# Kernel optimization log

Measured on AMD Instinct MI355X. Metric: run time of the kernel, lower is better.

The kernel has to match this reference:

```python
import jax, jax.numpy as jnp
import numpy as np

N = 100000   # subcomplex cells (nodes)
E = 600000   # edges in high-adjacency subcomplex graph
NB = 50000   # bridge (rank-0) cells
C = 128      # input_channels
H = 128      # hidden_channels
BN_EPS = 1e-5


def setup_inputs() -> dict:
    key = jax.random.key(0)
    ks = jax.random.split(key, 12)
    x = jax.random.normal(ks[0], (N, C), jnp.float32)
    x0 = jax.random.normal(ks[1], (NB, C), jnp.float32)
    edge_index = jax.random.randint(ks[2], (2, E), 0, N)
    bridge_index = jax.random.randint(ks[3], (E,), 0, NB)
    s1 = 1.0 / np.sqrt(C)
    s2 = 1.0 / np.sqrt(H)
    W1 = jax.random.uniform(ks[4], (C, H), jnp.float32, -s1, s1)
    b1 = jax.random.uniform(ks[5], (H,), jnp.float32, -s1, s1)
    W2 = jax.random.uniform(ks[6], (H, H), jnp.float32, -s2, s2)
    b2 = jax.random.uniform(ks[7], (H,), jnp.float32, -s2, s2)
    gamma1 = jnp.ones((H,), jnp.float32)
    beta1 = jnp.zeros((H,), jnp.float32)
    gamma2 = jnp.ones((H,), jnp.float32)
    beta2 = jnp.zeros((H,), jnp.float32)
    eps_gin = jnp.zeros((), jnp.float32)  # GIN train_eps, init 0
    return {"x": x, "x0": x0, "edge_index": edge_index, "bridge_index": bridge_index,
            "W1": W1, "b1": b1, "gamma1": gamma1, "beta1": beta1,
            "W2": W2, "b2": b2, "gamma2": gamma2, "beta2": beta2,
            "eps_gin": eps_gin}


def _bn(h, gamma, beta):
    # BatchNorm1d in training mode: batch stats over node dim, biased var
    mu = jnp.mean(h, axis=0)
    var = jnp.mean((h - mu) ** 2, axis=0)
    return gamma * (h - mu) * jax.lax.rsqrt(var + BN_EPS) + beta


def reference(x, x0, edge_index, bridge_index, W1, b1, gamma1, beta1,
              W2, b2, gamma2, beta2, eps_gin):
    src, dst = edge_index[0], edge_index[1]
    # edge attributes: gather bridge-cell features per edge  [E, C]
    edge_attr = x0[bridge_index]
    # GINE-style message: relu(x_j + e_ij), scatter-add into destination
    msg = jax.nn.relu(x[src] + edge_attr)
    aggr = jax.ops.segment_sum(msg, dst, num_segments=x.shape[0])  # [N, C]
    h = (1.0 + eps_gin) * x + aggr
    # 2-layer MLP: Linear -> BN -> ReLU, twice
    h = jax.nn.relu(_bn(h @ W1 + b1, gamma1, beta1))
    h = jax.nn.relu(_bn(h @ W2 + b2, gamma2, beta2))
    return h
```

## Files before the change

kernel.cpp:

```cpp
#include <hip/hip_runtime.h>


typedef __attribute__((ext_vector_type(8))) short bf16x8;
typedef __attribute__((ext_vector_type(4))) float floatx4;

__device__ __forceinline__ unsigned short f2bf(float f) {
  unsigned u = __float_as_uint(f);
  u += 0x7fff + ((u >> 16) & 1);
  return (unsigned short)(u >> 16);
}
__device__ __forceinline__ unsigned pk2(float a, float b) {
  return (unsigned)f2bf(a) | ((unsigned)f2bf(b) << 16);
}
__device__ __forceinline__ float bflo(unsigned u) { return __uint_as_float(u << 16); }
__device__ __forceinline__ float bfhi(unsigned u) { return __uint_as_float(u & 0xffff0000u); }

__global__ __launch_bounds__(256) void k_front(
    const float* __restrict__ x, const float* __restrict__ x0,
    const float* __restrict__ W1, const float* __restrict__ W2,
    unsigned short* __restrict__ WT1, unsigned short* __restrict__ WT2,
    uint4* __restrict__ zbase, int zitems, int zblocks,
    uint4* __restrict__ xb, int nx,
    uint4* __restrict__ x0b, int nx0) {
  int b = blockIdx.x;
  int tid = threadIdx.x;
  if (b < 2) {
    const float* W = b ? W2 : W1;
    unsigned short* WT = b ? WT2 : WT1;
#pragma unroll
    for (int i = 0; i < 16; ++i) {
      int g = tid + i * 256;
      int k = g >> 5;
      int n0 = (g & 31) * 4;
      float4 v = *(const float4*)(W + k * 128 + n0);
      WT[(n0 + 0) * 128 + k] = f2bf(v.x);
      WT[(n0 + 1) * 128 + k] = f2bf(v.y);
      WT[(n0 + 2) * 128 + k] = f2bf(v.z);
      WT[(n0 + 3) * 128 + k] = f2bf(v.w);
    }
    return;
  }
  if (b < 2 + zblocks) {
    int t = (b - 2) * 256 + tid;
    if (t < zitems) zbase[t] = make_uint4(0, 0, 0, 0);
    return;
  }
  int t = (b - 2 - zblocks) * 256 + tid;
  const float* s;
  uint4* d;
  if (t < nx) { s = x + (size_t)t * 8; d = xb + t; }
  else {
    t -= nx;
    if (t >= nx0) return;
    s = x0 + (size_t)t * 8; d = x0b + t;
  }
  float4 a = *(const float4*)s;
  float4 c = *(const float4*)(s + 4);
  uint4 o;
  o.x = pk2(a.x, a.y); o.y = pk2(a.z, a.w);
  o.z = pk2(c.x, c.y); o.w = pk2(c.z, c.w);
  *d = o;
}

__global__ __launch_bounds__(256) void k_scatter(
    const int* __restrict__ src, const int* __restrict__ dst,
    const int* __restrict__ bri, int* __restrict__ cnt,
    int2* __restrict__ slots, int E_) {
  int e = blockIdx.x * 256 + threadIdx.x;
  if (e >= E_) return;
  int d = dst[e];
  int pos = atomicAdd(&cnt[d], 1);
  if (pos < 32) slots[d * 32 + pos] = make_int2(src[e], bri[e]);
}

__global__ __launch_bounds__(256) void k_aggr(
    const uint4* __restrict__ xb, const uint4* __restrict__ x0b,
    const int* __restrict__ cnt, const int2* __restrict__ slots,
    const float* __restrict__ eps, uint4* __restrict__ aggr, int n) {
  int tid = threadIdx.x;
  int node = blockIdx.x * 32 + (tid >> 3);
  if (node >= n) return;
  int q = (tid & 7) + blockIdx.y * 8;
  float s = 1.0f + eps[0];
  float acc[8];
  uint4 xi = xb[(size_t)node * 16 + q];
  acc[0] = s * bflo(xi.x); acc[1] = s * bfhi(xi.x);
  acc[2] = s * bflo(xi.y); acc[3] = s * bfhi(xi.y);
  acc[4] = s * bflo(xi.z); acc[5] = s * bfhi(xi.z);
  acc[6] = s * bflo(xi.w); acc[7] = s * bfhi(xi.w);
  int end = cnt[node];
  if (end > 32) end = 32;
  int base = node * 32;
  for (int j = 0; j < end; ++j) {
    int2 p = slots[base + j];
    uint4 xa = xb[(size_t)p.x * 16 + q];
    uint4 ea = x0b[(size_t)p.y * 16 + q];
    acc[0] += fmaxf(bflo(xa.x) + bflo(ea.x), 0.f);
    acc[1] += fmaxf(bfhi(xa.x) + bfhi(ea.x), 0.f);
    acc[2] += fmaxf(bflo(xa.y) + bflo(ea.y), 0.f);
    acc[3] += fmaxf(bfhi(xa.y) + bfhi(ea.y), 0.f);
    acc[4] += fmaxf(bflo(xa.z) + bflo(ea.z), 0.f);
    acc[5] += fmaxf(bfhi(xa.z) + bfhi(ea.z), 0.f);
    acc[6] += fmaxf(bflo(xa.w) + bflo(ea.w), 0.f);
    acc[7] += fmaxf(bfhi(xa.w) + bfhi(ea.w), 0.f);
  }
  uint4 o;
  o.x = pk2(acc[0], acc[1]); o.y = pk2(acc[2], acc[3]);
  o.z = pk2(acc[4], acc[5]); o.w = pk2(acc[6], acc[7]);
  aggr[(size_t)node * 16 + q] = o;
}

__global__ __launch_bounds__(256) void k_gemmb(
    const unsigned short* A, const unsigned short* __restrict__ WT,
    const float* __restrict__ bias,
    const float* __restrict__ psum, const float* __restrict__ psq,
    const float* __restrict__ gam, const float* __restrict__ bet,
    unsigned short* Out,
    float* __restrict__ osum, float* __restrict__ osq,
    int nrows, float inv_n, int fuse) {
  __shared__ unsigned short LDSraw[128 * 144];
  unsigned short* As = LDSraw;
  unsigned short* Bs = LDSraw + 128 * 72;
  __shared__ float sL[128], hL[128];
  int tid = threadIdx.x;
  if (fuse && tid < 128) {
    float mu = psum[tid] * inv_n;
    float var = psq[tid] * inv_n - mu * mu;
    float rs = rsqrtf(var + 1e-5f);
    float sc = gam[tid] * rs;
    sL[tid] = sc;
    hL[tid] = bet[tid] - mu * sc;
  }
  __syncthreads();

  int row0 = blockIdx.x * 128;
  int lane = tid & 63;
  int wid = tid >> 6;
  int wr = (wid >> 1) * 64;
  int wc = (wid & 1) * 64;
  int lr = lane & 15;
  int quad = lane >> 4;

  floatx4 acc[4][4];
#pragma unroll
  for (int mi = 0; mi < 4; ++mi)
#pragma unroll
    for (int ni = 0; ni < 4; ++ni) acc[mi][ni] = (floatx4)0.0f;

  for (int kc = 0; kc < 128; kc += 64) {
    if (kc) __syncthreads();
#pragma unroll
    for (int i = 0; i < 4; ++i) {
      int g = tid + i * 256;
      int r = g >> 3;
      int c8 = g & 7;
      int row = row0 + r;
      uint4 v = make_uint4(0, 0, 0, 0);
      if (row < nrows)
        v = *(const uint4*)(A + (size_t)row * 128 + kc + c8 * 8);
      if (fuse) {
        int k = kc + c8 * 8;
        v.x = pk2(fmaxf(fmaf(sL[k + 0], bflo(v.x), hL[k + 0]), 0.f),
                  fmaxf(fmaf(sL[k + 1], bfhi(v.x), hL[k + 1]), 0.f));
        v.y = pk2(fmaxf(fmaf(sL[k + 2], bflo(v.y), hL[k + 2]), 0.f),
                  fmaxf(fmaf(sL[k + 3], bfhi(v.y), hL[k + 3]), 0.f));
        v.z = pk2(fmaxf(fmaf(sL[k + 4], bflo(v.z), hL[k + 4]), 0.f),
                  fmaxf(fmaf(sL[k + 5], bfhi(v.z), hL[k + 5]), 0.f));
        v.w = pk2(fmaxf(fmaf(sL[k + 6], bflo(v.w), hL[k + 6]), 0.f),
                  fmaxf(fmaf(sL[k + 7], bfhi(v.w), hL[k + 7]), 0.f));
      }
      *(uint4*)&As[r * 72 + c8 * 8] = v;
    }
#pragma unroll
    for (int i = 0; i < 4; ++i) {
      int g = tid + i * 256;
      int nn = g >> 3;
      int c8 = g & 7;
      *(uint4*)&Bs[nn * 72 + c8 * 8] =
          *(const uint4*)(WT + (size_t)nn * 128 + kc + c8 * 8);
    }
    __syncthreads();
#pragma unroll
    for (int ks = 0; ks < 2; ++ks) {
      int k0 = ks * 32 + quad * 8;
      bf16x8 af[4], bfr[4];
#pragma unroll
      for (int mi = 0; mi < 4; ++mi)
        af[mi] = *(const bf16x8*)&As[(wr + mi * 16 + lr) * 72 + k0];
#pragma unroll
      for (int ni = 0; ni < 4; ++ni)
        bfr[ni] = *(const bf16x8*)&Bs[(wc + ni * 16 + lr) * 72 + k0];
#pragma unroll
      for (int mi = 0; mi < 4; ++mi)
#pragma unroll
        for (int ni = 0; ni < 4; ++ni)
          acc[mi][ni] = __builtin_amdgcn_mfma_f32_16x16x32_bf16(
              af[mi], bfr[ni], acc[mi][ni], 0, 0, 0);
    }
  }
  __syncthreads();

  float bv[4];
#pragma unroll
  for (int ni = 0; ni < 4; ++ni) bv[ni] = bias[wc + ni * 16 + lr];
  float s_sum[4] = {0.f, 0.f, 0.f, 0.f};
  float s_sq[4]  = {0.f, 0.f, 0.f, 0.f};
#pragma unroll
  for (int mi = 0; mi < 4; ++mi) {
#pragma unroll
    for (int r = 0; r < 4; ++r) {
      int rl = wr + mi * 16 + quad * 4 + r;
      bool ok = (row0 + rl) < nrows;
#pragma unroll
      for (int ni = 0; ni < 4; ++ni) {
        int col = wc + ni * 16 + lr;
        float v = acc[mi][ni][r] + bv[ni];
        LDSraw[rl * 136 + col] = f2bf(v);
        if (ok) { s_sum[ni] += v; s_sq[ni] += v * v; }
      }
    }
  }
#pragma unroll
  for (int ni = 0; ni < 4; ++ni) {
    s_sum[ni] += __shfl_xor(s_sum[ni], 16, 64);
    s_sum[ni] += __shfl_xor(s_sum[ni], 32, 64);
    s_sq[ni]  += __shfl_xor(s_sq[ni], 16, 64);
    s_sq[ni]  += __shfl_xor(s_sq[ni], 32, 64);
  }
  if (quad == 0) {
#pragma unroll
    for (int ni = 0; ni < 4; ++ni) {
      int col = wc + ni * 16 + lr;
      unsafeAtomicAdd(&osum[col], s_sum[ni]);
      unsafeAtomicAdd(&osq[col], s_sq[ni]);
    }
  }
  __syncthreads();
#pragma unroll
  for (int i = 0; i < 8; ++i) {
    int g = tid + i * 256;
    int r = g >> 4;
    int c8 = g & 15;
    if (row0 + r < nrows)
      *(uint4*)(Out + (size_t)(row0 + r) * 128 + c8 * 8) =
          *(const uint4*)&LDSraw[r * 136 + c8 * 8];
  }
}

__global__ __launch_bounds__(256) void k_bnrelu(
    const uint4* __restrict__ h, const float* __restrict__ psum,
    const float* __restrict__ psq, const float* __restrict__ gam,
    const float* __restrict__ bet, float* __restrict__ out,
    int items, float inv_n) {
  __shared__ float sL[128], hL[128];
  int tid = threadIdx.x;
  if (tid < 128) {
    float mu = psum[tid] * inv_n;
    float var = psq[tid] * inv_n - mu * mu;
    float rs = rsqrtf(var + 1e-5f);
    float sc = gam[tid] * rs;
    sL[tid] = sc;
    hL[tid] = bet[tid] - mu * sc;
  }
  __syncthreads();
  int t = blockIdx.x * 256 + tid;
  if (t >= items) return;
  int c = (t & 15) * 8;
  uint4 v = h[t];
  float4 o1, o2;
  o1.x = fmaxf(fmaf(sL[c + 0], bflo(v.x), hL[c + 0]), 0.f);
  o1.y = fmaxf(fmaf(sL[c + 1], bfhi(v.x), hL[c + 1]), 0.f);
  o1.z = fmaxf(fmaf(sL[c + 2], bflo(v.y), hL[c + 2]), 0.f);
  o1.w = fmaxf(fmaf(sL[c + 3], bfhi(v.y), hL[c + 3]), 0.f);
  o2.x = fmaxf(fmaf(sL[c + 4], bflo(v.z), hL[c + 4]), 0.f);
  o2.y = fmaxf(fmaf(sL[c + 5], bfhi(v.z), hL[c + 5]), 0.f);
  o2.z = fmaxf(fmaf(sL[c + 6], bflo(v.w), hL[c + 6]), 0.f);
  o2.w = fmaxf(fmaf(sL[c + 7], bfhi(v.w), hL[c + 7]), 0.f);
  ((float4*)out)[(size_t)t * 2 + 0] = o1;
  ((float4*)out)[(size_t)t * 2 + 1] = o2;
}

extern "C" void kernel_launch(void* const* d_in, const int* in_sizes, int n_in,
                              void* d_out, int out_size, void* d_ws, size_t ws_size,
                              hipStream_t stream) {
  const float* x   = (const float*)d_in[0];
  const float* x0  = (const float*)d_in[1];
  const int*   ei  = (const int*)d_in[2];
  const int*   bi  = (const int*)d_in[3];
  const float* W1  = (const float*)d_in[4];
  const float* b1  = (const float*)d_in[5];
  const float* g1  = (const float*)d_in[6];
  const float* be1 = (const float*)d_in[7];
  const float* W2  = (const float*)d_in[8];
  const float* b2  = (const float*)d_in[9];
  const float* g2  = (const float*)d_in[10];
  const float* be2 = (const float*)d_in[11];
  const float* eps = (const float*)d_in[12];

  int N  = in_sizes[0] / 128;
  int NB = in_sizes[1] / 128;
  int E_ = in_sizes[3];
  const int* srcp = ei;
  const int* dstp = ei + E_;

  int2* slots = (int2*)d_ws;
  int* cnt    = (int*)(slots + (size_t)N * 32);
  float* stats = (float*)(cnt + N);
  float* sum1 = stats;       float* sq1 = stats + 128;
  float* sum2 = stats + 256; float* sq2 = stats + 384;
  unsigned short* WT1  = (unsigned short*)(stats + 512);
  unsigned short* WT2  = WT1 + 16384;
  unsigned short* abuf = WT2 + 16384;

  unsigned short* xb  = (unsigned short*)d_out;
  unsigned short* x0b = xb + (size_t)N * 128;

  int zitems  = (N + 512 + 3) / 4;
  int zblocks = (zitems + 255) / 256;
  int nx  = N * 16;
  int nx0 = NB * 16;
  int cvtblocks = (nx + nx0 + 255) / 256;
  float inv_n = 1.0f / (float)N;

  k_front<<<2 + zblocks + cvtblocks, 256, 0, stream>>>(
      x, x0, W1, W2, WT1, WT2, (uint4*)cnt, zitems, zblocks,
      (uint4*)xb, nx, (uint4*)x0b, nx0);

  k_scatter<<<(E_ + 255) / 256, 256, 0, stream>>>(srcp, dstp, bi, cnt,
                                                  slots, E_);

  dim3 agrid((N * 8 + 255) / 256, 2);
  k_aggr<<<agrid, 256, 0, stream>>>(
      (const uint4*)xb, (const uint4*)x0b, cnt, slots, eps,
      (uint4*)abuf, N);

  int gblocks = (N + 127) / 128;
  k_gemmb<<<gblocks, 256, 0, stream>>>(abuf, WT1, b1, nullptr, nullptr,
                                       nullptr, nullptr, abuf, sum1, sq1,
                                       N, inv_n, 0);
  k_gemmb<<<gblocks, 256, 0, stream>>>(abuf, WT2, b2, sum1, sq1, g1, be1,
                                       abuf, sum2, sq2, N, inv_n, 1);

  k_bnrelu<<<(N * 16 + 255) / 256, 256, 0, stream>>>(
      (const uint4*)abuf, sum2, sq2, g2, be2, (float*)d_out, N * 16, inv_n);
}
```

Measured before the change: 343.6 us.

## Fuse all stages into one persistent cooperative kernel with grid syncs

Replaces the six separate launches (convert/zero, scatter, aggregate, two GEMMs, final BN-ReLU) with one cooperative persistent kernel. The kernel loops over work with grid-stride and separates phases with grid.sync(). The goal is to remove launch gaps and tail effects between small kernels. In exchange, grid size is capped by occupancy, each phase loses some parallelism, and every phase boundary pays a grid-wide barrier. The aggregation also changes from two half-row blocks to 16 threads per node.

```diff
diff --git a/kernel.cpp b/kernel.cpp
--- a/kernel.cpp
+++ b/kernel.cpp
@@ -1,4 +1,7 @@
 #include <hip/hip_runtime.h>
+#include <hip/hip_cooperative_groups.h>
+
+namespace cg = cooperative_groups;
 
 
 typedef __attribute__((ext_vector_type(8))) short bf16x8;
@@ -15,125 +18,31 @@
 __device__ __forceinline__ float bflo(unsigned u) { return __uint_as_float(u << 16); }
 __device__ __forceinline__ float bfhi(unsigned u) { return __uint_as_float(u & 0xffff0000u); }
 
-__global__ __launch_bounds__(256) void k_front(
-    const float* __restrict__ x, const float* __restrict__ x0,
-    const float* __restrict__ W1, const float* __restrict__ W2,
-    unsigned short* __restrict__ WT1, unsigned short* __restrict__ WT2,
-    uint4* __restrict__ zbase, int zitems, int zblocks,
-    uint4* __restrict__ xb, int nx,
-    uint4* __restrict__ x0b, int nx0) {
-  int b = blockIdx.x;
-  int tid = threadIdx.x;
-  if (b < 2) {
-    const float* W = b ? W2 : W1;
-    unsigned short* WT = b ? WT2 : WT1;
-#pragma unroll
-    for (int i = 0; i < 16; ++i) {
-      int g = tid + i * 256;
-      int k = g >> 5;
-      int n0 = (g & 31) * 4;
-      float4 v = *(const float4*)(W + k * 128 + n0);
-      WT[(n0 + 0) * 128 + k] = f2bf(v.x);
-      WT[(n0 + 1) * 128 + k] = f2bf(v.y);
-      WT[(n0 + 2) * 128 + k] = f2bf(v.z);
-      WT[(n0 + 3) * 128 + k] = f2bf(v.w);
-    }
-    return;
-  }
-  if (b < 2 + zblocks) {
-    int t = (b - 2) * 256 + tid;
-    if (t < zitems) zbase[t] = make_uint4(0, 0, 0, 0);
-    return;
-  }
-  int t = (b - 2 - zblocks) * 256 + tid;
-  const float* s;
-  uint4* d;
-  if (t < nx) { s = x + (size_t)t * 8; d = xb + t; }
-  else {
-    t -= nx;
-    if (t >= nx0) return;
-    s = x0 + (size_t)t * 8; d = x0b + t;
-  }
-  float4 a = *(const float4*)s;
-  float4 c = *(const float4*)(s + 4);
-  uint4 o;
-  o.x = pk2(a.x, a.y); o.y = pk2(a.z, a.w);
-  o.z = pk2(c.x, c.y); o.w = pk2(c.z, c.w);
-  *d = o;
-}
-
-__global__ __launch_bounds__(256) void k_scatter(
-    const int* __restrict__ src, const int* __restrict__ dst,
-    const int* __restrict__ bri, int* __restrict__ cnt,
-    int2* __restrict__ slots, int E_) {
-  int e = blockIdx.x * 256 + threadIdx.x;
-  if (e >= E_) return;
-  int d = dst[e];
-  int pos = atomicAdd(&cnt[d], 1);
-  if (pos < 32) slots[d * 32 + pos] = make_int2(src[e], bri[e]);
-}
-
-__global__ __launch_bounds__(256) void k_aggr(
-    const uint4* __restrict__ xb, const uint4* __restrict__ x0b,
-    const int* __restrict__ cnt, const int2* __restrict__ slots,
-    const float* __restrict__ eps, uint4* __restrict__ aggr, int n) {
-  int tid = threadIdx.x;
-  int node = blockIdx.x * 32 + (tid >> 3);
-  if (node >= n) return;
-  int q = (tid & 7) + blockIdx.y * 8;
-  float s = 1.0f + eps[0];
-  float acc[8];
-  uint4 xi = xb[(size_t)node * 16 + q];
-  acc[0] = s * bflo(xi.x); acc[1] = s * bfhi(xi.x);
-  acc[2] = s * bflo(xi.y); acc[3] = s * bfhi(xi.y);
-  acc[4] = s * bflo(xi.z); acc[5] = s * bfhi(xi.z);
-  acc[6] = s * bflo(xi.w); acc[7] = s * bfhi(xi.w);
-  int end = cnt[node];
-  if (end > 32) end = 32;
-  int base = node * 32;
-  for (int j = 0; j < end; ++j) {
-    int2 p = slots[base + j];
-    uint4 xa = xb[(size_t)p.x * 16 + q];
-    uint4 ea = x0b[(size_t)p.y * 16 + q];
-    acc[0] += fmaxf(bflo(xa.x) + bflo(ea.x), 0.f);
-    acc[1] += fmaxf(bfhi(xa.x) + bfhi(ea.x), 0.f);
-    acc[2] += fmaxf(bflo(xa.y) + bflo(ea.y), 0.f);
-    acc[3] += fmaxf(bfhi(xa.y) + bfhi(ea.y), 0.f);
-    acc[4] += fmaxf(bflo(xa.z) + bflo(ea.z), 0.f);
-    acc[5] += fmaxf(bfhi(xa.z) + bfhi(ea.z), 0.f);
-    acc[6] += fmaxf(bflo(xa.w) + bflo(ea.w), 0.f);
-    acc[7] += fmaxf(bfhi(xa.w) + bfhi(ea.w), 0.f);
-  }
-  uint4 o;
-  o.x = pk2(acc[0], acc[1]); o.y = pk2(acc[2], acc[3]);
-  o.z = pk2(acc[4], acc[5]); o.w = pk2(acc[6], acc[7]);
-  aggr[(size_t)node * 16 + q] = o;
-}
-
-__global__ __launch_bounds__(256) void k_gemmb(
-    const unsigned short* A, const unsigned short* __restrict__ WT,
-    const float* __restrict__ bias,
-    const float* __restrict__ psum, const float* __restrict__ psq,
-    const float* __restrict__ gam, const float* __restrict__ bet,
-    unsigned short* Out,
-    float* __restrict__ osum, float* __restrict__ osq,
-    int nrows, float inv_n, int fuse) {
-  __shared__ unsigned short LDSraw[128 * 144];
+struct MegaParams {
+  const float *x, *x0;
+  const int *src, *dst, *bri;
+  const float *W1, *b1, *g1, *be1;
+  const float *W2, *b2, *g2, *be2;
+  const float *eps;
+  unsigned short *xb, *x0b, *WT1, *WT2, *abuf;
+  int2 *slots;
+  int *cnt;
+  float *stats;
+  uint4 *zbase;
+  int zitems;
+  float *out;
+  int N, NB, E;
+  float inv_n;
+};
+
+__device__ __forceinline__ void gemm_tile(
+    int t, int tid, const unsigned short* A, const unsigned short* WT,
+    const float* bias, unsigned short* Out, float* osum, float* osq,
+    int nrows, unsigned short* LDSraw, const float* sL, const float* hL,
+    int fuse) {
   unsigned short* As = LDSraw;
   unsigned short* Bs = LDSraw + 128 * 72;
-  __shared__ float sL[128], hL[128];
-  int tid = threadIdx.x;
-  if (fuse && tid < 128) {
-    float mu = psum[tid] * inv_n;
-    float var = psq[tid] * inv_n - mu * mu;
-    float rs = rsqrtf(var + 1e-5f);
-    float sc = gam[tid] * rs;
-    sL[tid] = sc;
-    hL[tid] = bet[tid] - mu * sc;
-  }
-  __syncthreads();
-
-  int row0 = blockIdx.x * 128;
+  int row0 = t << 7;
   int lane = tid & 63;
   int wid = tid >> 6;
   int wr = (wid >> 1) * 64;
@@ -147,8 +56,9 @@
 #pragma unroll
     for (int ni = 0; ni < 4; ++ni) acc[mi][ni] = (floatx4)0.0f;
 
+#pragma unroll
   for (int kc = 0; kc < 128; kc += 64) {
-    if (kc) __syncthreads();
+    __syncthreads();
 #pragma unroll
     for (int i = 0; i < 4; ++i) {
       int g = tid + i * 256;
@@ -247,13 +157,10 @@
   }
 }
 
-__global__ __launch_bounds__(256) void k_bnrelu(
-    const uint4* __restrict__ h, const float* __restrict__ psum,
-    const float* __restrict__ psq, const float* __restrict__ gam,
-    const float* __restrict__ bet, float* __restrict__ out,
-    int items, float inv_n) {
-  __shared__ float sL[128], hL[128];
-  int tid = threadIdx.x;
+__device__ __forceinline__ void fold_bn(int tid, const float* psum,
+                                        const float* psq, const float* gam,
+                                        const float* bet, float inv_n,
+                                        float* sL, float* hL) {
   if (tid < 128) {
     float mu = psum[tid] * inv_n;
     float var = psq[tid] * inv_n - mu * mu;
@@ -262,85 +169,170 @@
     sL[tid] = sc;
     hL[tid] = bet[tid] - mu * sc;
   }
+}
+
+__global__ __launch_bounds__(256, 3) void k_mega(MegaParams p) {
+  cg::grid_group grid = cg::this_grid();
+  __shared__ unsigned short LDSraw[128 * 144];
+  __shared__ float sL[128], hL[128];
+  int tid = threadIdx.x;
+  int gid = blockIdx.x * 256 + tid;
+  int gsize = gridDim.x * 256;
+
+  for (int i = gid; i < p.zitems; i += gsize) p.zbase[i] = make_uint4(0, 0, 0, 0);
+  int nx = p.N * 16;
+  for (int i = gid; i < nx; i += gsize) {
+    const float* s = p.x + (size_t)i * 8;
+    float4 a = *(const float4*)s;
+    float4 c = *(const float4*)(s + 4);
+    uint4 o;
+    o.x = pk2(a.x, a.y); o.y = pk2(a.z, a.w);
+    o.z = pk2(c.x, c.y); o.w = pk2(c.z, c.w);
+    ((uint4*)p.xb)[i] = o;
+  }
+  int nx0 = p.NB * 16;
+  for (int i = gid; i < nx0; i += gsize) {
+    const float* s = p.x0 + (size_t)i * 8;
+    float4 a = *(const float4*)s;
+    float4 c = *(const float4*)(s + 4);
+    uint4 o;
+    o.x = pk2(a.x, a.y); o.y = pk2(a.z, a.w);
+    o.z = pk2(c.x, c.y); o.w = pk2(c.z, c.w);
+    ((uint4*)p.x0b)[i] = o;
+  }
+  for (int i = gid; i < 8192; i += gsize) {
+    const float* W = (i & 4096) ? p.W2 : p.W1;
+    unsigned short* WT = (i & 4096) ? p.WT2 : p.WT1;
+    int r = i & 4095;
+    int k = r >> 5;
+    int n0 = (r & 31) * 4;
+    float4 v = *(const float4*)(W + k * 128 + n0);
+    WT[(n0 + 0) * 128 + k] = f2bf(v.x);
+    WT[(n0 + 1) * 128 + k] = f2bf(v.y);
+    WT[(n0 + 2) * 128 + k] = f2bf(v.z);
+    WT[(n0 + 3) * 128 + k] = f2bf(v.w);
+  }
+  grid.sync();
+
+  for (int e = gid; e < p.E; e += gsize) {
+    int d = p.dst[e];
+    int pos = atomicAdd(&p.cnt[d], 1);
+    if (pos < 32) p.slots[d * 32 + pos] = make_int2(p.src[e], p.bri[e]);
+  }
+  grid.sync();
+
+  {
+    float epsv = 1.0f + p.eps[0];
+    int q = tid & 15;
+    int ngroups = gsize >> 4;
+    for (int n = (gid >> 4); n < p.N; n += ngroups) {
+      uint4 xi = ((const uint4*)p.xb)[(size_t)n * 16 + q];
+      float acc[8];
+      acc[0] = epsv * bflo(xi.x); acc[1] = epsv * bfhi(xi.x);
+      acc[2] = epsv * bflo(xi.y); acc[3] = epsv * bfhi(xi.y);
+      acc[4] = epsv * bflo(xi.z); acc[5] = epsv * bfhi(xi.z);
+      acc[6] = epsv * bflo(xi.w); acc[7] = epsv * bfhi(xi.w);
+      int end = p.cnt[n];
+      if (end > 32) end = 32;
+      const int2* sl = p.slots + n * 32;
+      for (int j = 0; j < end; ++j) {
+        int2 pr = sl[j];
+        uint4 xa = ((const uint4*)p.xb)[(size_t)pr.x * 16 + q];
+        uint4 ea = ((const uint4*)p.x0b)[(size_t)pr.y * 16 + q];
+        acc[0] += fmaxf(bflo(xa.x) + bflo(ea.x), 0.f);
+        acc[1] += fmaxf(bfhi(xa.x) + bfhi(ea.x), 0.f);
+        acc[2] += fmaxf(bflo(xa.y) + bflo(ea.y), 0.f);
+        acc[3] += fmaxf(bfhi(xa.y) + bfhi(ea.y), 0.f);
+        acc[4] += fmaxf(bflo(xa.z) + bflo(ea.z), 0.f);
+        acc[5] += fmaxf(bfhi(xa.z) + bfhi(ea.z), 0.f);
+        acc[6] += fmaxf(bflo(xa.w) + bflo(ea.w), 0.f);
+        acc[7] += fmaxf(bfhi(xa.w) + bfhi(ea.w), 0.f);
+      }
+      uint4 o;
+      o.x = pk2(acc[0], acc[1]); o.y = pk2(acc[2], acc[3]);
+      o.z = pk2(acc[4], acc[5]); o.w = pk2(acc[6], acc[7]);
+      ((uint4*)p.abuf)[(size_t)n * 16 + q] = o;
+    }
+  }
+  grid.sync();
+
+  int ntiles = (p.N + 127) >> 7;
+  for (int t = blockIdx.x; t < ntiles; t += gridDim.x)
+    gemm_tile(t, tid, p.abuf, p.WT1, p.b1, p.abuf,
+              p.stats + 0, p.stats + 128, p.N, LDSraw, nullptr, nullptr, 0);
+  grid.sync();
+
+  fold_bn(tid, p.stats + 0, p.stats + 128, p.g1, p.be1, p.inv_n, sL, hL);
   __syncthreads();
-  int t = blockIdx.x * 256 + tid;
-  if (t >= items) return;
-  int c = (t & 15) * 8;
-  uint4 v = h[t];
-  float4 o1, o2;
-  o1.x = fmaxf(fmaf(sL[c + 0], bflo(v.x), hL[c + 0]), 0.f);
-  o1.y = fmaxf(fmaf(sL[c + 1], bfhi(v.x), hL[c + 1]), 0.f);
-  o1.z = fmaxf(fmaf(sL[c + 2], bflo(v.y), hL[c + 2]), 0.f);
-  o1.w = fmaxf(fmaf(sL[c + 3], bfhi(v.y), hL[c + 3]), 0.f);
-  o2.x = fmaxf(fmaf(sL[c + 4], bflo(v.z), hL[c + 4]), 0.f);
-  o2.y = fmaxf(fmaf(sL[c + 5], bfhi(v.z), hL[c + 5]), 0.f);
-  o2.z = fmaxf(fmaf(sL[c + 6], bflo(v.w), hL[c + 6]), 0.f);
-  o2.w = fmaxf(fmaf(sL[c + 7], bfhi(v.w), hL[c + 7]), 0.f);
-  ((float4*)out)[(size_t)t * 2 + 0] = o1;
-  ((float4*)out)[(size_t)t * 2 + 1] = o2;
+  for (int t = blockIdx.x; t < ntiles; t += gridDim.x)
+    gemm_tile(t, tid, p.abuf, p.WT2, p.b2, p.abuf,
+              p.stats + 256, p.stats + 384, p.N, LDSraw, sL, hL, 1);
+  grid.sync();
+
+  fold_bn(tid, p.stats + 256, p.stats + 384, p.g2, p.be2, p.inv_n, sL, hL);
+  __syncthreads();
+  for (int i = gid; i < nx; i += gsize) {
+    uint4 v = ((const uint4*)p.abuf)[i];
+    int c = (i & 15) * 8;
+    float4 o1, o2;
+    o1.x = fmaxf(fmaf(sL[c + 0], bflo(v.x), hL[c + 0]), 0.f);
+    o1.y = fmaxf(fmaf(sL[c + 1], bfhi(v.x), hL[c + 1]), 0.f);
+    o1.z = fmaxf(fmaf(sL[c + 2], bflo(v.y), hL[c + 2]), 0.f);
+    o1.w = fmaxf(fmaf(sL[c + 3], bfhi(v.y), hL[c + 3]), 0.f);
+    o2.x = fmaxf(fmaf(sL[c + 4], bflo(v.z), hL[c + 4]), 0.f);
+    o2.y = fmaxf(fmaf(sL[c + 5], bfhi(v.z), hL[c + 5]), 0.f);
+    o2.z = fmaxf(fmaf(sL[c + 6], bflo(v.w), hL[c + 6]), 0.f);
+    o2.w = fmaxf(fmaf(sL[c + 7], bfhi(v.w), hL[c + 7]), 0.f);
+    ((float4*)p.out)[(size_t)i * 2 + 0] = o1;
+    ((float4*)p.out)[(size_t)i * 2 + 1] = o2;
+  }
 }
 
 extern "C" void kernel_launch(void* const* d_in, const int* in_sizes, int n_in,
                               void* d_out, int out_size, void* d_ws, size_t ws_size,
                               hipStream_t stream) {
-  const float* x   = (const float*)d_in[0];
-  const float* x0  = (const float*)d_in[1];
-  const int*   ei  = (const int*)d_in[2];
-  const int*   bi  = (const int*)d_in[3];
-  const float* W1  = (const float*)d_in[4];
-  const float* b1  = (const float*)d_in[5];
-  const float* g1  = (const float*)d_in[6];
-  const float* be1 = (const float*)d_in[7];
-  const float* W2  = (const float*)d_in[8];
-  const float* b2  = (const float*)d_in[9];
-  const float* g2  = (const float*)d_in[10];
-  const float* be2 = (const float*)d_in[11];
-  const float* eps = (const float*)d_in[12];
-
-  int N  = in_sizes[0] / 128;
-  int NB = in_sizes[1] / 128;
-  int E_ = in_sizes[3];
-  const int* srcp = ei;
-  const int* dstp = ei + E_;
-
-  int2* slots = (int2*)d_ws;
-  int* cnt    = (int*)(slots + (size_t)N * 32);
-  float* stats = (float*)(cnt + N);
-  float* sum1 = stats;       float* sq1 = stats + 128;
-  float* sum2 = stats + 256; float* sq2 = stats + 384;
-  unsigned short* WT1  = (unsigned short*)(stats + 512);
-  unsigned short* WT2  = WT1 + 16384;
-  unsigned short* abuf = WT2 + 16384;
-
-  unsigned short* xb  = (unsigned short*)d_out;
-  unsigned short* x0b = xb + (size_t)N * 128;
-
-  int zitems  = (N + 512 + 3) / 4;
-  int zblocks = (zitems + 255) / 256;
-  int nx  = N * 16;
-  int nx0 = NB * 16;
-  int cvtblocks = (nx + nx0 + 255) / 256;
-  float inv_n = 1.0f / (float)N;
-
-  k_front<<<2 + zblocks + cvtblocks, 256, 0, stream>>>(
-      x, x0, W1, W2, WT1, WT2, (uint4*)cnt, zitems, zblocks,
-      (uint4*)xb, nx, (uint4*)x0b, nx0);
-
-  k_scatter<<<(E_ + 255) / 256, 256, 0, stream>>>(srcp, dstp, bi, cnt,
-                                                  slots, E_);
-
-  dim3 agrid((N * 8 + 255) / 256, 2);
-  k_aggr<<<agrid, 256, 0, stream>>>(
-      (const uint4*)xb, (const uint4*)x0b, cnt, slots, eps,
-      (uint4*)abuf, N);
-
-  int gblocks = (N + 127) / 128;
-  k_gemmb<<<gblocks, 256, 0, stream>>>(abuf, WT1, b1, nullptr, nullptr,
-                                       nullptr, nullptr, abuf, sum1, sq1,
-                                       N, inv_n, 0);
-  k_gemmb<<<gblocks, 256, 0, stream>>>(abuf, WT2, b2, sum1, sq1, g1, be1,
-                                       abuf, sum2, sq2, N, inv_n, 1);
-
-  k_bnrelu<<<(N * 16 + 255) / 256, 256, 0, stream>>>(
-      (const uint4*)abuf, sum2, sq2, g2, be2, (float*)d_out, N * 16, inv_n);
-}
+  MegaParams p;
+  p.x   = (const float*)d_in[0];
+  p.x0  = (const float*)d_in[1];
+  const int* ei = (const int*)d_in[2];
+  p.bri = (const int*)d_in[3];
+  p.W1  = (const float*)d_in[4];
+  p.b1  = (const float*)d_in[5];
+  p.g1  = (const float*)d_in[6];
+  p.be1 = (const float*)d_in[7];
+  p.W2  = (const float*)d_in[8];
+  p.b2  = (const float*)d_in[9];
+  p.g2  = (const float*)d_in[10];
+  p.be2 = (const float*)d_in[11];
+  p.eps = (const float*)d_in[12];
+
+  p.N  = in_sizes[0] / 128;
+  p.NB = in_sizes[1] / 128;
+  p.E  = in_sizes[3];
+  p.src = ei;
+  p.dst = ei + p.E;
+  p.inv_n = 1.0f / (float)p.N;
+
+  p.slots = (int2*)d_ws;
+  p.cnt   = (int*)(p.slots + (size_t)p.N * 32);
+  p.stats = (float*)(p.cnt + p.N);
+  p.WT1   = (unsigned short*)(p.stats + 512);
+  p.WT2   = p.WT1 + 16384;
+  p.abuf  = p.WT2 + 16384;
+  p.zbase = (uint4*)p.cnt;
+  p.zitems = (p.N + 512) / 4;
+
+  p.xb  = (unsigned short*)d_out;
+  p.x0b = p.xb + (size_t)p.N * 128;
+  p.out = (float*)d_out;
+
+  int occ = 0;
+  hipOccupancyMaxActiveBlocksPerMultiprocessor(&occ, (const void*)k_mega, 256, 0);
+  if (occ < 1) occ = 1;
+  if (occ > 4) occ = 4;
+  int grid = occ * 256;
+
+  void* args[] = {&p};
+  hipLaunchCooperativeKernel((const void*)k_mega, dim3(grid), dim3(256),
+                             args, 0, stream);
+}
```

Result: slower. 634.7 us (+84.7%).
